# Optimization experiments

Measured on AMD Instinct MI355X. Metric: run time of the kernel, lower is better.

The kernel has to match this reference:

```python
import jax, jax.numpy as jnp
import numpy as np
from jax import lax

B, N, NCAM, NLVL = 2, 65536, 5, 3
CIN, MID, OUT, PTSC = 256, 128, 128, 128
H, W = 64, 112
EPS = 1e-3


def setup_inputs() -> dict:
    ks = jax.random.split(jax.random.key(0), 8)
    f32 = jnp.float32
    img_feats = jax.random.normal(ks[0], (NLVL, B * NCAM, CIN, H, W), f32)
    # points roughly in front of the cameras (z ~ 15) so many project in-bounds
    pts_xyz = jax.random.normal(ks[1], (B, N, 3), f32) * 10.0 + jnp.array([0.0, 0.0, 15.0], f32)
    cam_ids = jnp.sort(jax.random.randint(ks[2], (B, N), 0, NCAM), axis=1).astype(jnp.int32)
    pts_feats = jax.random.normal(ks[3], (B * N, PTSC), f32)
    T = jnp.broadcast_to(jnp.eye(4, dtype=f32), (NCAM, 4, 4))
    T = T.at[:, :3, 3].set(jax.random.normal(ks[4], (NCAM, 3), f32) * 0.5)
    fx, fy, cx, cy = 400.0, 400.0, 4.0 * W, 4.0 * H  # full-res intrinsics (feature stride 8)
    K = jnp.broadcast_to(jnp.array([[fx, 0.0, cx], [0.0, fy, cy], [0.0, 0.0, 1.0]], f32), (NCAM, 3, 3))
    conv_w = jax.random.normal(ks[5], (NLVL, MID, CIN, 3, 3), f32) * 0.02
    conv_b = jnp.zeros((NLVL, MID), f32)
    img_w = jax.random.normal(ks[6], (OUT, MID * NLVL), f32) * 0.05
    img_b = jnp.zeros((OUT,), f32)
    img_gamma = jnp.ones((OUT,), f32)
    img_beta = jnp.zeros((OUT,), f32)
    pts_w = jax.random.normal(ks[7], (OUT, PTSC), f32) * 0.05
    pts_b = jnp.zeros((OUT,), f32)
    pts_gamma = jnp.ones((OUT,), f32)
    pts_beta = jnp.zeros((OUT,), f32)
    return dict(img_feats=img_feats, pts_xyz=pts_xyz, pts_feats=pts_feats, T=T, K=K,
                conv_w=conv_w, conv_b=conv_b, img_w=img_w, img_b=img_b,
                img_gamma=img_gamma, img_beta=img_beta, pts_w=pts_w, pts_b=pts_b,
                pts_gamma=pts_gamma, pts_beta=pts_beta, cam_ids=cam_ids)


def _bn(x, gamma, beta):
    # BatchNorm1d in training mode: batch statistics, biased variance, eps=1e-3
    mu = jnp.mean(x, axis=0)
    var = jnp.var(x, axis=0)
    return (x - mu) * lax.rsqrt(var + EPS) * gamma + beta


def _bilinear(feat, bidx, cam, px, py):
    # feat: [B, NCAM, H, W, C]; px/py: [B, N] pixel coords (align_corners=True)
    # grid_sample bilinear with zeros padding: out-of-bounds corners contribute 0
    x0f = jnp.floor(px)
    y0f = jnp.floor(py)
    wx1 = px - x0f
    wy1 = py - y0f

    def corner(xf, yf, wgt):
        valid = (xf >= 0) & (xf <= W - 1) & (yf >= 0) & (yf <= H - 1)
        xi = jnp.clip(xf, 0, W - 1).astype(jnp.int32)
        yi = jnp.clip(yf, 0, H - 1).astype(jnp.int32)
        v = feat[bidx, cam, yi, xi]  # [B, N, C]
        return v * (wgt * valid)[..., None]

    return (corner(x0f, y0f, (1 - wx1) * (1 - wy1))
            + corner(x0f + 1, y0f, wx1 * (1 - wy1))
            + corner(x0f, y0f + 1, (1 - wx1) * wy1)
            + corner(x0f + 1, y0f + 1, wx1 * wy1))


def _forward(img_feats, pts_xyz, pts_feats, T, K, conv_w, conv_b, img_w, img_b,
             img_gamma, img_beta, pts_w, pts_b, pts_gamma, pts_beta, cam_ids):
    # scale intrinsics to the 1/8-resolution feature maps (K[0,0],K[0,2],K[1,1],K[1,2] /= 8)
    k_scale = jnp.array([[0.125, 1.0, 0.125], [1.0, 0.125, 0.125], [1.0, 1.0, 1.0]], jnp.float32)
    Ks = K * k_scale
    ones = jnp.ones(pts_xyz.shape[:2] + (1,), pts_xyz.dtype)
    xyz1 = jnp.concatenate([pts_xyz, ones], axis=-1)      # [B, N, 4]
    Tc = T[cam_ids]                                        # [B, N, 4, 4]
    Kc = Ks[cam_ids]                                       # [B, N, 3, 3]
    pc = jnp.einsum('bnij,bnj->bni', Tc, xyz1)[..., :3]    # camera-frame coords
    pim = jnp.einsum('bnij,bnj->bni', Kc, pc)
    uv = pim[..., :2] / pim[..., 2:3]
    gx = uv[..., 0] / W * 2.0 - 1.0                        # normalized grid coords
    gy = uv[..., 1] / H * 2.0 - 1.0
    px = (gx + 1.0) * 0.5 * (W - 1)                        # align_corners=True mapping
    py = (gy + 1.0) * 0.5 * (H - 1)
    bidx = jnp.broadcast_to(jnp.arange(B)[:, None], cam_ids.shape)
    lvl_feats = []
    for l in range(NLVL):
        f = lax.conv_general_dilated(img_feats[l], conv_w[l], (1, 1), 'SAME',
                                     dimension_numbers=('NCHW', 'OIHW', 'NCHW'))
        f = f + conv_b[l][None, :, None, None]
        f = f.reshape(B, NCAM, MID, H, W).transpose(0, 1, 3, 4, 2)  # [B,NCAM,H,W,C]
        lvl_feats.append(_bilinear(f, bidx, cam_ids, px, py))       # [B,N,MID]
    img_pts = jnp.concatenate(lvl_feats, axis=-1).reshape(B * N, MID * NLVL)
    img_pre = _bn(img_pts @ img_w.T + img_b, img_gamma, img_beta)
    pts_pre = _bn(pts_feats @ pts_w.T + pts_b, pts_gamma, pts_beta)
    return jax.nn.relu(img_pre + pts_pre)


def reference(img_feats, pts_xyz, pts_feats, T, K, conv_w, conv_b, img_w, img_b,
              img_gamma, img_beta, pts_w, pts_b, pts_gamma, pts_beta, cam_ids):
    return _forward(img_feats, pts_xyz, pts_feats, T, K, conv_w, conv_b, img_w, img_b,
                    img_gamma, img_beta, pts_w, pts_b, pts_gamma, pts_beta, cam_ids)
```

## Files before the change

kernel.cpp:

```cpp
#include <hip/hip_runtime.h>
#include <cstdint>

#define LVLPOS 75240
#define GUARD  256
#define NPART  16

using f32x4  = __attribute__((ext_vector_type(4))) float;
using bf16x8 = __attribute__((ext_vector_type(8))) __bf16;

static __device__ __forceinline__ unsigned short f2bf(float f) {
  unsigned int u = __float_as_uint(f);
  u += 0x7fffu + ((u >> 16) & 1u);
  return (unsigned short)(u >> 16);
}
static __device__ __forceinline__ float bflo(uint32_t d) { return __uint_as_float(d << 16); }
static __device__ __forceinline__ float bfhi(uint32_t d) { return __uint_as_float(d & 0xffff0000u); }

#define OFF_WF     ((size_t)0)
#define OFF_BIAS   ((size_t)1769472)
#define OFF_PTSWB  ((size_t)1769984)
#define OFF_STATSP ((size_t)1802752)
#define OFF_FDAT   ((size_t)1835520)
#define OFF_IMGP   ((size_t)21103104)
#define OFF_IRAW   OFF_IMGP
#define OFF_PRAW   (OFF_IMGP + (size_t)33554432)

__global__ __launch_bounds__(256) void k_setup(const float* __restrict__ img_w,
                                               const float* __restrict__ conv_w,
                                               const float* __restrict__ conv_b,
                                               const float* __restrict__ pts_w,
                                               unsigned short* __restrict__ wf,
                                               float* __restrict__ bias,
                                               unsigned short* __restrict__ pts_wb,
                                               unsigned short* __restrict__ imgP,
                                               float* __restrict__ statsP) {
  __shared__ float smem[12544];
  const int b = blockIdx.x, t = threadIdx.x;
  if (b < 432) {
    int z = b >> 1, oh = b & 1;
    int l = z / 72, r = z % 72, tap = r / 8, ckk = r % 8;
    float* iw = smem;
    float* cw = smem + 8320;
    for (int v = t; v < 2048; v += 256) {
      int o = v >> 5, seg = v & 31;
      float4 f = *(const float4*)(img_w + (size_t)(oh * 64 + o) * 384 + l * 128 + seg * 4);
      float* d = iw + o * 130 + seg * 4;
      d[0] = f.x; d[1] = f.y; d[2] = f.z; d[3] = f.w;
    }
    for (int v = t; v < 4096; v += 256) {
      int mid = v >> 5, cj = v & 31;
      cw[mid * 33 + cj] = conv_w[(size_t)((l * 128 + mid) * 256 + ckk * 32 + cj) * 9 + tap];
    }
    __syncthreads();
    const int o64 = t & 63, cs = t >> 6, o = oh * 64 + o64;
    float accs[8];
    #pragma unroll
    for (int ci = 0; ci < 8; ++ci) accs[ci] = 0.f;
    for (int mid = 0; mid < 128; ++mid) {
      float a = iw[o64 * 130 + mid];
      #pragma unroll
      for (int ci = 0; ci < 8; ++ci) accs[ci] = fmaf(a, cw[mid * 33 + cs * 8 + ci], accs[ci]);
    }
    #pragma unroll
    for (int ci = 0; ci < 8; ++ci) {
      int c = ckk * 32 + cs * 8 + ci;
      int ck64 = c >> 6, c64 = c & 63;
      int kh = c64 >> 5, kq3 = (c64 >> 3) & 3, el = c64 & 7;
      size_t idx = (size_t)((l * 4 + ck64) * 9 + tap) * 8192
                 + (size_t)(((o >> 4) * 2 + kh) * 512) + ((o & 15) + 16 * kq3) * 8 + el;
      wf[idx] = f2bf(accs[ci]);
    }
  } else if (b < 494) {
    int z = b - 432;
    size_t base; int n16;
    if (z == 60)      { base = 0; n16 = 8192; }
    else if (z == 61) { base = (size_t)(GUARD + 3 * LVLPOS) * 256; n16 = 8192; }
    else {
      int lvl = z / 20, w = z % 20, n = w >> 1, y = (w & 1) ? 65 : 0;
      base = (size_t)(GUARD + lvl * LVLPOS + (n * 66 + y) * 114) * 256; n16 = 3648;
    }
    uint4 zz = {0u, 0u, 0u, 0u};
    uint4* d = (uint4*)(imgP + base);
    for (int v = t; v < n16; v += 256) d[v] = zz;
  } else if (b < 559) {
    int z = b - 494;
    if (z == 0) {
      if (t < 128) {
        float a = 0.f;
        for (int i = 0; i < 384; ++i) a = fmaf(img_w[t * 384 + i], conv_b[i], a);
        bias[t] = a;
      }
    } else {
      int idx = (z - 1) * 256 + t;
      int o = idx >> 7, k = idx & 127;
      int ks = k >> 5, kq = (k >> 3) & 3, el = k & 7;
      int pos = (ks * 8 + (o >> 4)) * 512 + ((o & 15) + 16 * kq) * 8 + el;
      pts_wb[pos] = f2bf(pts_w[idx]);
    }
  } else {
    int z = b - 559;
    ((float4*)statsP)[z * 256 + t] = (float4){0.f, 0.f, 0.f, 0.f};
  }
}

__global__ __launch_bounds__(256) void k_nhwc(const float* __restrict__ img,
                                              unsigned short* __restrict__ imgP) {
  __shared__ unsigned short tile[256 * 114];
  const int t = threadIdx.x;
  const int lvl = blockIdx.x / 640, r = blockIdx.x % 640, n = r >> 6, y = r & 63;
  const float4* src4 = (const float4*)(img + (size_t)(lvl * 10 + n) * 1835008 + (size_t)y * 112);
  for (int v = t; v < 7168; v += 256) {
    int c = v / 28, s = v - c * 28;
    float4 f = src4[(size_t)c * 1792 + s];
    uint2 d;
    d.x = (uint32_t)f2bf(f.x) | ((uint32_t)f2bf(f.y) << 16);
    d.y = (uint32_t)f2bf(f.z) | ((uint32_t)f2bf(f.w) << 16);
    *(uint2*)(tile + c * 114 + s * 4) = d;
  }
  __syncthreads();
  uint32_t* dst = (uint32_t*)(imgP + (size_t)(GUARD + lvl * LVLPOS + (n * 66 + y + 1) * 114) * 256);
  for (int v = t; v < 14592; v += 256) {
    int xp = v >> 7, cp = v & 127;
    uint32_t val = 0;
    if (xp >= 1 && xp <= 112) {
      int x = xp - 1;
      val = (uint32_t)tile[(2 * cp) * 114 + x] | ((uint32_t)tile[(2 * cp + 1) * 114 + x] << 16);
    }
    dst[v] = val;
  }
}

#define APITCH 72
static __device__ __forceinline__ void conv_stage(unsigned short* dst,
                                                  const unsigned short* __restrict__ imgP,
                                                  int s, int m0, int t) {
  int lvl = s / 12, r = s - lvl * 12;
  int ck = r / 3, ky = r - ck * 3;
  const unsigned short* base = imgP
      + (size_t)(GUARD + lvl * LVLPOS + m0 - 1 + (ky - 1) * 114) * 256 + ck * 64;
  for (int v = t; v < 528; v += 256) {
    int p = v >> 3, seg = v & 7;
    *(uint4*)(dst + p * APITCH + seg * 8) = *(const uint4*)(base + (size_t)p * 256 + seg * 8);
  }
}

static __device__ __forceinline__ void conv_compute(const unsigned short* As_,
                                                    const unsigned short* __restrict__ wf,
                                                    int s, int mh, int nh, int m, int kq,
                                                    f32x4 (&acc)[2][4]) {
  const unsigned short* W0 = wf + (size_t)(3 * s) * 8192 + (nh * 8) * 512 + (m + 16 * kq) * 8;
  #pragma unroll
  for (int kx = 0; kx < 3; ++kx) {
    const unsigned short* Wp = W0 + kx * 8192;
    bf16x8 bv[4][2];
    #pragma unroll
    for (int nt = 0; nt < 4; ++nt) {
      bv[nt][0] = *(const bf16x8*)(Wp + (nt * 2) * 512);
      bv[nt][1] = *(const bf16x8*)(Wp + (nt * 2 + 1) * 512);
    }
    #pragma unroll
    for (int mt = 0; mt < 2; ++mt) {
      const unsigned short* ap = As_ + (mh * 32 + mt * 16 + m + kx) * APITCH + kq * 8;
      bf16x8 a0 = *(const bf16x8*)(ap);
      bf16x8 a1 = *(const bf16x8*)(ap + 32);
      #pragma unroll
      for (int nt = 0; nt < 4; ++nt) {
        acc[mt][nt] = __builtin_amdgcn_mfma_f32_16x16x32_bf16(a0, bv[nt][0], acc[mt][nt], 0, 0, 0);
        acc[mt][nt] = __builtin_amdgcn_mfma_f32_16x16x32_bf16(a1, bv[nt][1], acc[mt][nt], 0, 0, 0);
      }
    }
  }
}

__global__ __launch_bounds__(256, 4) void k_conv(const unsigned short* __restrict__ imgP,
                                                 const unsigned short* __restrict__ wf,
                                                 const float* __restrict__ bias,
                                                 unsigned short* __restrict__ fdat) {
  __shared__ unsigned short As[2][66 * APITCH];
  const int t = threadIdx.x, lane = t & 63, wave = t >> 6;
  const int mh = wave & 1, nh = wave >> 1;
  const int m = lane & 15, kq = lane >> 4;
  const int m0 = blockIdx.x * 64;

  f32x4 acc[2][4];
  #pragma unroll
  for (int i = 0; i < 2; ++i)
    #pragma unroll
    for (int j = 0; j < 4; ++j) acc[i][j] = (f32x4){0.f, 0.f, 0.f, 0.f};

  conv_stage(As[0], imgP, 0, m0, t);
  #pragma unroll 1
  for (int s = 0; s < 36; s += 2) {
    __syncthreads();
    if (s + 1 < 36) conv_stage(As[1], imgP, s + 1, m0, t);
    conv_compute(As[0], wf, s, mh, nh, m, kq, acc);
    __syncthreads();
    if (s + 2 < 36) conv_stage(As[0], imgP, s + 2, m0, t);
    conv_compute(As[1], wf, s + 1, mh, nh, m, kq, acc);
  }
  __syncthreads();

  unsigned short* Ep = &As[0][0];
  #pragma unroll
  for (int nt = 0; nt < 4; ++nt) {
    int oc = nh * 64 + nt * 16 + m;
    float bv = bias[oc];
    #pragma unroll
    for (int mt = 0; mt < 2; ++mt)
      #pragma unroll
      for (int rr = 0; rr < 4; ++rr)
        Ep[(mh * 32 + mt * 16 + kq * 4 + rr) * 128 + oc] = f2bf(acc[mt][nt][rr] + bv);
  }
  __syncthreads();
  unsigned short* dst = fdat + (size_t)m0 * 128;
  for (int v = t; v < 1024; v += 256)
    *(uint4*)(dst + v * 8) = *(const uint4*)(Ep + v * 8);
}

__global__ __launch_bounds__(256) void k_gp(const float* __restrict__ pts_xyz,
                                            const int* __restrict__ cam_ids,
                                            const float* __restrict__ Tm,
                                            const float* __restrict__ Km,
                                            const unsigned short* __restrict__ fdat,
                                            const float* __restrict__ pts_feats,
                                            const unsigned short* __restrict__ pts_wb,
                                            unsigned short* __restrict__ img_raw,
                                            unsigned short* __restrict__ pts_raw,
                                            float* __restrict__ statsP) {
  __shared__ __align__(16) char smem[36864];
  const int t = threadIdx.x, lane = t & 63, wave = t >> 6;

  if (blockIdx.x < 8192) {
    float* sb = (float*)smem;
    float* qb = sb + 128;
    if (t < 128) { sb[t] = 0.f; sb[128 + t] = 0.f; }
    __syncthreads();
    const int p0 = blockIdx.x * 16 + wave * 4;
    const uint32_t* fq = (const uint32_t*)fdat;
    float s0 = 0.f, q0 = 0.f, s1 = 0.f, q1 = 0.f;
    for (int j = 0; j < 4; ++j) {
      const int p = p0 + j;
      const int b = p >> 16;
      const int cam = cam_ids[p];
      const float X = pts_xyz[(size_t)p * 3], Y = pts_xyz[(size_t)p * 3 + 1], Z = pts_xyz[(size_t)p * 3 + 2];
      const float* Tc = Tm + cam * 16;
      float pcx = Tc[0] * X + Tc[1] * Y + Tc[2]  * Z + Tc[3];
      float pcy = Tc[4] * X + Tc[5] * Y + Tc[6]  * Z + Tc[7];
      float pcz = Tc[8] * X + Tc[9] * Y + Tc[10] * Z + Tc[11];
      const float* Kc = Km + cam * 9;
      float pimx = Kc[0] * 0.125f * pcx + Kc[1] * pcy          + Kc[2] * 0.125f * pcz;
      float pimy = Kc[3] * pcx          + Kc[4] * 0.125f * pcy + Kc[5] * 0.125f * pcz;
      float pimz = Kc[6] * pcx          + Kc[7] * pcy          + Kc[8] * pcz;
      float u = pimx / pimz, vv = pimy / pimz;
      float px = (u / 112.f) * 111.f;
      float py = (vv / 64.f) * 63.f;
      float x0 = floorf(px), y0 = floorf(py);
      float wx = px - x0, wy = py - y0;
      float cxf[4] = {x0, x0 + 1.f, x0, x0 + 1.f};
      float cyf[4] = {y0, y0, y0 + 1.f, y0 + 1.f};
      float cwt[4] = {(1.f - wx) * (1.f - wy), wx * (1.f - wy), (1.f - wx) * wy, wx * wy};
      const int nimg = b * 5 + cam;
      float wv[4]; int idx[4]; bool any = false;
      #pragma unroll
      for (int c4 = 0; c4 < 4; ++c4) {
        float xf = cxf[c4], yf = cyf[c4];
        bool valid = (xf >= 0.f) && (xf <= 111.f) && (yf >= 0.f) && (yf <= 63.f);
        float w = cwt[c4] * (valid ? 1.f : 0.f);
        int xi = (int)fminf(fmaxf(xf, 0.f), 111.f);
        int yi = (int)fminf(fmaxf(yf, 0.f), 63.f);
        wv[c4] = w;
        idx[c4] = (nimg * 66 + yi + 1) * 114 + xi + 1;
        any = any || (w != 0.f);
      }
      float a0 = 0.f, a1 = 0.f;
      if (any) {
        #pragma unroll
        for (int c4 = 0; c4 < 4; ++c4) {
          uint32_t d = fq[(size_t)idx[c4] * 64 + lane];
          a0 = fmaf(wv[c4], bflo(d), a0);
          a1 = fmaf(wv[c4], bfhi(d), a1);
        }
      }
      s0 += a0; q0 += a0 * a0; s1 += a1; q1 += a1 * a1;
      ((uint32_t*)img_raw)[(size_t)p * 64 + lane] =
          (uint32_t)f2bf(a0) | ((uint32_t)f2bf(a1) << 16);
    }
    atomicAdd(&sb[lane * 2], s0);
    atomicAdd(&sb[lane * 2 + 1], s1);
    atomicAdd(&qb[lane * 2], q0);
    atomicAdd(&qb[lane * 2 + 1], q1);
    __syncthreads();
    if (t < 128) {
      float* sp = statsP + (size_t)(blockIdx.x & (NPART - 1)) * 512;
      atomicAdd(sp + t, sb[t]);
      atomicAdd(sp + 128 + t, qb[t]);
    }
  } else {
    const int pb = blockIdx.x - 8192;
    const size_t r0 = (size_t)pb * 128;
    unsigned short* As2 = (unsigned short*)smem;
    const int mh = wave & 1, nh = wave >> 1;
    const int m = lane & 15, kq = lane >> 4;
    for (int v = t; v < 4096; v += 256) {
      int mm = v >> 5, seg = v & 31;
      float4 f = *(const float4*)(pts_feats + (r0 + mm) * 128 + seg * 4);
      uint2 d;
      d.x = (uint32_t)f2bf(f.x) | ((uint32_t)f2bf(f.y) << 16);
      d.y = (uint32_t)f2bf(f.z) | ((uint32_t)f2bf(f.w) << 16);
      *(uint2*)(As2 + mm * 136 + seg * 4) = d;
    }
    __syncthreads();
    f32x4 acc[4][4];
    #pragma unroll
    for (int i = 0; i < 4; ++i)
      #pragma unroll
      for (int jj = 0; jj < 4; ++jj) acc[i][jj] = (f32x4){0.f, 0.f, 0.f, 0.f};
    #pragma unroll
    for (int ks = 0; ks < 4; ++ks) {
      bf16x8 bv[4];
      #pragma unroll
      for (int nt = 0; nt < 4; ++nt)
        bv[nt] = *(const bf16x8*)(pts_wb + (size_t)((ks * 8 + nh * 4 + nt) * 512) + lane * 8);
      #pragma unroll
      for (int mt = 0; mt < 4; ++mt) {
        bf16x8 af = *(const bf16x8*)(As2 + (mh * 64 + mt * 16 + m) * 136 + ks * 32 + kq * 8);
        #pragma unroll
        for (int nt = 0; nt < 4; ++nt)
          acc[mt][nt] = __builtin_amdgcn_mfma_f32_16x16x32_bf16(af, bv[nt], acc[mt][nt], 0, 0, 0);
      }
    }
    __syncthreads();
    #pragma unroll
    for (int mt = 0; mt < 4; ++mt)
      #pragma unroll
      for (int nt = 0; nt < 4; ++nt)
        #pragma unroll
        for (int rr = 0; rr < 4; ++rr)
          As2[(mh * 64 + mt * 16 + kq * 4 + rr) * 128 + nh * 64 + nt * 16 + m] = f2bf(acc[mt][nt][rr]);
    __syncthreads();
    unsigned short* dst = pts_raw + r0 * 128;
    for (int v = t; v < 2048; v += 256)
      *(uint4*)(dst + v * 8) = *(const uint4*)(As2 + v * 8);
    float* ps = (float*)(smem + 34816);
    float* pq = ps + 256;
    pq = (float*)(smem + 35840);
    {
      int col = t & 127, rh = t >> 7;
      float s = 0.f, q = 0.f;
      for (int i = 0; i < 64; ++i) {
        float v = __uint_as_float((uint32_t)As2[(rh * 64 + i) * 128 + col] << 16);
        s += v; q += v * v;
      }
      ps[rh * 128 + col] = s;
      pq[rh * 128 + col] = q;
    }
    __syncthreads();
    if (t < 128) {
      float* sp = statsP + (size_t)(blockIdx.x & (NPART - 1)) * 512;
      atomicAdd(sp + 256 + t, ps[t] + ps[128 + t]);
      atomicAdd(sp + 384 + t, pq[t] + pq[128 + t]);
    }
  }
}

__global__ __launch_bounds__(256) void k_final(const unsigned short* __restrict__ img_raw,
                                               const unsigned short* __restrict__ pts_raw,
                                               const float* __restrict__ statsP,
                                               const float* __restrict__ img_gamma,
                                               const float* __restrict__ img_beta,
                                               const float* __restrict__ pts_gamma,
                                               const float* __restrict__ pts_beta,
                                               float* __restrict__ out) {
  __shared__ float sA[128], sB[128], sC[128];
  const int t = threadIdx.x;
  if (t < 128) {
    float si = 0.f, qi = 0.f, sp = 0.f, qp = 0.f;
    for (int k = 0; k < NPART; ++k) {
      const float* st = statsP + (size_t)k * 512;
      si += st[t]; qi += st[128 + t]; sp += st[256 + t]; qp += st[384 + t];
    }
    const float Nr = 131072.f;
    float mu_i = si / Nr;
    float var_i = qi / Nr - mu_i * mu_i;
    float a_i = img_gamma[t] * rsqrtf(var_i + 1e-3f);
    float mu_p = sp / Nr;
    float var_p = qp / Nr - mu_p * mu_p;
    float a_p = pts_gamma[t] * rsqrtf(var_p + 1e-3f);
    sA[t] = a_i; sB[t] = a_p;
    sC[t] = img_beta[t] + pts_beta[t] - a_i * mu_i - a_p * mu_p;
  }
  __syncthreads();
  const uint32_t* ir = (const uint32_t*)img_raw;
  const uint32_t* pr = (const uint32_t*)pts_raw;
  size_t g0 = (size_t)blockIdx.x * 2048;
  for (int i = 0; i < 8; ++i) {
    size_t g = g0 + i * 256 + t;
    uint32_t di = ir[g], dp = pr[g];
    int c = (int)(g & 63) * 2;
    float o0 = fmaxf(0.f, sA[c] * bflo(di) + sB[c] * bflo(dp) + sC[c]);
    float o1 = fmaxf(0.f, sA[c + 1] * bfhi(di) + sB[c + 1] * bfhi(dp) + sC[c + 1]);
    float2 o; o.x = o0; o.y = o1;
    *(float2*)(out + g * 2) = o;
  }
}

extern "C" void kernel_launch(void* const* d_in, const int* in_sizes, int n_in,
                              void* d_out, int out_size, void* d_ws, size_t ws_size,
                              hipStream_t stream) {
  const float* img_feats = (const float*)d_in[0];
  const float* pts_xyz   = (const float*)d_in[1];
  const float* pts_feats = (const float*)d_in[2];
  const float* Tm        = (const float*)d_in[3];
  const float* Km        = (const float*)d_in[4];
  const float* conv_w    = (const float*)d_in[5];
  const float* conv_b    = (const float*)d_in[6];
  const float* img_w     = (const float*)d_in[7];
  const float* img_gamma = (const float*)d_in[9];
  const float* img_beta  = (const float*)d_in[10];
  const float* pts_w     = (const float*)d_in[11];
  const float* pts_gamma = (const float*)d_in[13];
  const float* pts_beta  = (const float*)d_in[14];
  const int*   cam_ids   = (const int*)d_in[15];

  char* wsb = (char*)d_ws;
  unsigned short* wf      = (unsigned short*)(wsb + OFF_WF);
  float*          bias    = (float*)(wsb + OFF_BIAS);
  unsigned short* pts_wb  = (unsigned short*)(wsb + OFF_PTSWB);
  float*          statsP  = (float*)(wsb + OFF_STATSP);
  unsigned short* fdat    = (unsigned short*)(wsb + OFF_FDAT);
  unsigned short* imgP    = (unsigned short*)(wsb + OFF_IMGP);
  unsigned short* img_raw = (unsigned short*)(wsb + OFF_IRAW);
  unsigned short* pts_raw = (unsigned short*)(wsb + OFF_PRAW);

  k_setup<<<dim3(567), dim3(256), 0, stream>>>(img_w, conv_w, conv_b, pts_w,
                                               wf, bias, pts_wb, imgP, statsP);
  k_nhwc<<<dim3(1920), dim3(256), 0, stream>>>(img_feats, imgP);
  k_conv<<<dim3(1176), dim3(256), 0, stream>>>(imgP, wf, bias, fdat);
  k_gp<<<dim3(9216), dim3(256), 0, stream>>>(pts_xyz, cam_ids, Tm, Km, fdat,
                                             pts_feats, pts_wb, img_raw, pts_raw, statsP);
  k_final<<<dim3(4096), dim3(256), 0, stream>>>(img_raw, pts_raw, statsP,
                                                img_gamma, img_beta, pts_gamma, pts_beta,
                                                (float*)d_out);
}
```

Before: 742.3 us.

## Split conv per level with 128-row tiles and LDS-staged weights

The 3x3 conv kernel now gives each block a single level and 128 output rows, instead of accumulating all three levels into 64 rows. Weights are staged into double-buffered LDS with global_load_lds, so the MFMA loop reads B from shared memory rather than global. Per-level conv outputs and biases are now stored separately, and the gather kernel sums the three levels while sampling, which triples the gather read traffic and the fdat workspace. The NHWC transpose is split into channel halves using a padded 32-bit LDS tile, and the stats atomics in the gather are moved inside the per-point loop.

```diff
diff --git a/kernel.cpp b/kernel.cpp
--- a/kernel.cpp
+++ b/kernel.cpp
@@ -4,6 +4,7 @@
 #define LVLPOS 75240
 #define GUARD  256
 #define NPART  16
+#define FLVL32 4816896
 
 using f32x4  = __attribute__((ext_vector_type(4))) float;
 using bf16x8 = __attribute__((ext_vector_type(8))) __bf16;
@@ -16,12 +17,23 @@
 static __device__ __forceinline__ float bflo(uint32_t d) { return __uint_as_float(d << 16); }
 static __device__ __forceinline__ float bfhi(uint32_t d) { return __uint_as_float(d & 0xffff0000u); }
 
+#if __has_builtin(__builtin_amdgcn_global_load_lds)
+#define HAVE_GLL 1
+typedef const __attribute__((address_space(1))) unsigned int* gas1_t;
+typedef __attribute__((address_space(3))) unsigned int* las3_t;
+static __device__ __forceinline__ void gll16(const void* g, void* l) {
+  __builtin_amdgcn_global_load_lds((gas1_t)g, (las3_t)l, 16, 0, 0);
+}
+#else
+#define HAVE_GLL 0
+#endif
+
 #define OFF_WF     ((size_t)0)
 #define OFF_BIAS   ((size_t)1769472)
-#define OFF_PTSWB  ((size_t)1769984)
-#define OFF_STATSP ((size_t)1802752)
-#define OFF_FDAT   ((size_t)1835520)
-#define OFF_IMGP   ((size_t)21103104)
+#define OFF_PTSWB  ((size_t)1771008)
+#define OFF_STATSP ((size_t)1803776)
+#define OFF_FDAT   ((size_t)1836544)
+#define OFF_IMGP   ((size_t)59639296)
 #define OFF_IRAW   OFF_IMGP
 #define OFF_PRAW   (OFF_IMGP + (size_t)33554432)
 
@@ -86,9 +98,12 @@
     int z = b - 494;
     if (z == 0) {
       if (t < 128) {
-        float a = 0.f;
-        for (int i = 0; i < 384; ++i) a = fmaf(img_w[t * 384 + i], conv_b[i], a);
-        bias[t] = a;
+        for (int l = 0; l < 3; ++l) {
+          float a = 0.f;
+          for (int mid = 0; mid < 128; ++mid)
+            a = fmaf(img_w[t * 384 + l * 128 + mid], conv_b[l * 128 + mid], a);
+          bias[l * 128 + t] = a;
+        }
       }
     } else {
       int idx = (z - 1) * 256 + t;
@@ -105,115 +120,131 @@
 
 __global__ __launch_bounds__(256) void k_nhwc(const float* __restrict__ img,
                                               unsigned short* __restrict__ imgP) {
-  __shared__ unsigned short tile[256 * 114];
+  __shared__ uint32_t tile32[7280];
   const int t = threadIdx.x;
-  const int lvl = blockIdx.x / 640, r = blockIdx.x % 640, n = r >> 6, y = r & 63;
-  const float4* src4 = (const float4*)(img + (size_t)(lvl * 10 + n) * 1835008 + (size_t)y * 112);
-  for (int v = t; v < 7168; v += 256) {
-    int c = v / 28, s = v - c * 28;
-    float4 f = src4[(size_t)c * 1792 + s];
-    uint2 d;
-    d.x = (uint32_t)f2bf(f.x) | ((uint32_t)f2bf(f.y) << 16);
-    d.y = (uint32_t)f2bf(f.z) | ((uint32_t)f2bf(f.w) << 16);
-    *(uint2*)(tile + c * 114 + s * 4) = d;
+  const int lvl = blockIdx.x / 1280;
+  const int r = blockIdx.x % 1280;
+  const int n = r >> 7, w = r & 127, y = w >> 1, half = w & 1;
+  const float4* src4 = (const float4*)(img + (size_t)(lvl * 10 + n) * 1835008
+                                       + (size_t)(half * 128) * 7168 + (size_t)y * 112);
+  for (int v = t; v < 1792; v += 256) {
+    int s = v % 28, a = v / 28;
+    float4 f0 = src4[(size_t)(2 * a) * 1792 + s];
+    float4 f1 = src4[(size_t)(2 * a + 1) * 1792 + s];
+    uint32_t* dst = tile32 + (4 * s) * 65 + a;
+    dst[0]      = (uint32_t)f2bf(f0.x) | ((uint32_t)f2bf(f1.x) << 16);
+    dst[65]     = (uint32_t)f2bf(f0.y) | ((uint32_t)f2bf(f1.y) << 16);
+    dst[130]    = (uint32_t)f2bf(f0.z) | ((uint32_t)f2bf(f1.z) << 16);
+    dst[195]    = (uint32_t)f2bf(f0.w) | ((uint32_t)f2bf(f1.w) << 16);
   }
   __syncthreads();
-  uint32_t* dst = (uint32_t*)(imgP + (size_t)(GUARD + lvl * LVLPOS + (n * 66 + y + 1) * 114) * 256);
-  for (int v = t; v < 14592; v += 256) {
-    int xp = v >> 7, cp = v & 127;
+  uint32_t* dst32 = (uint32_t*)(imgP + (size_t)(GUARD + lvl * LVLPOS + (n * 66 + y + 1) * 114) * 256)
+                  + half * 64;
+  for (int v = t; v < 7296; v += 256) {
+    int xp = v >> 6, a = v & 63;
     uint32_t val = 0;
-    if (xp >= 1 && xp <= 112) {
-      int x = xp - 1;
-      val = (uint32_t)tile[(2 * cp) * 114 + x] | ((uint32_t)tile[(2 * cp + 1) * 114 + x] << 16);
-    }
-    dst[v] = val;
-  }
-}
-
-#define APITCH 72
-static __device__ __forceinline__ void conv_stage(unsigned short* dst,
-                                                  const unsigned short* __restrict__ imgP,
-                                                  int s, int m0, int t) {
-  int lvl = s / 12, r = s - lvl * 12;
-  int ck = r / 3, ky = r - ck * 3;
-  const unsigned short* base = imgP
-      + (size_t)(GUARD + lvl * LVLPOS + m0 - 1 + (ky - 1) * 114) * 256 + ck * 64;
-  for (int v = t; v < 528; v += 256) {
-    int p = v >> 3, seg = v & 7;
-    *(uint4*)(dst + p * APITCH + seg * 8) = *(const uint4*)(base + (size_t)p * 256 + seg * 8);
-  }
-}
-
-static __device__ __forceinline__ void conv_compute(const unsigned short* As_,
-                                                    const unsigned short* __restrict__ wf,
-                                                    int s, int mh, int nh, int m, int kq,
-                                                    f32x4 (&acc)[2][4]) {
-  const unsigned short* W0 = wf + (size_t)(3 * s) * 8192 + (nh * 8) * 512 + (m + 16 * kq) * 8;
-  #pragma unroll
-  for (int kx = 0; kx < 3; ++kx) {
-    const unsigned short* Wp = W0 + kx * 8192;
-    bf16x8 bv[4][2];
-    #pragma unroll
-    for (int nt = 0; nt < 4; ++nt) {
-      bv[nt][0] = *(const bf16x8*)(Wp + (nt * 2) * 512);
-      bv[nt][1] = *(const bf16x8*)(Wp + (nt * 2 + 1) * 512);
-    }
-    #pragma unroll
-    for (int mt = 0; mt < 2; ++mt) {
-      const unsigned short* ap = As_ + (mh * 32 + mt * 16 + m + kx) * APITCH + kq * 8;
-      bf16x8 a0 = *(const bf16x8*)(ap);
-      bf16x8 a1 = *(const bf16x8*)(ap + 32);
-      #pragma unroll
-      for (int nt = 0; nt < 4; ++nt) {
-        acc[mt][nt] = __builtin_amdgcn_mfma_f32_16x16x32_bf16(a0, bv[nt][0], acc[mt][nt], 0, 0, 0);
-        acc[mt][nt] = __builtin_amdgcn_mfma_f32_16x16x32_bf16(a1, bv[nt][1], acc[mt][nt], 0, 0, 0);
-      }
-    }
-  }
-}
-
-__global__ __launch_bounds__(256, 4) void k_conv(const unsigned short* __restrict__ imgP,
+    if (xp >= 1 && xp <= 112) val = tile32[(xp - 1) * 65 + a];
+    dst32[(size_t)xp * 128 + a] = val;
+  }
+}
+
+__global__ __launch_bounds__(256, 3) void k_conv(const unsigned short* __restrict__ imgP,
                                                  const unsigned short* __restrict__ wf,
                                                  const float* __restrict__ bias,
                                                  unsigned short* __restrict__ fdat) {
-  __shared__ unsigned short As[2][66 * APITCH];
+  __shared__ unsigned short lds[9360 + 2 * 8192];
+  unsigned short* As = lds;
+  unsigned short* Bs = lds + 9360;
   const int t = threadIdx.x, lane = t & 63, wave = t >> 6;
   const int mh = wave & 1, nh = wave >> 1;
   const int m = lane & 15, kq = lane >> 4;
-  const int m0 = blockIdx.x * 64;
-
-  f32x4 acc[2][4];
+  const int lvl = blockIdx.x / 588;
+  const int m0 = (blockIdx.x % 588) * 128;
+
+  f32x4 acc[4][4];
   #pragma unroll
-  for (int i = 0; i < 2; ++i)
+  for (int i = 0; i < 4; ++i)
     #pragma unroll
     for (int j = 0; j < 4; ++j) acc[i][j] = (f32x4){0.f, 0.f, 0.f, 0.f};
 
-  conv_stage(As[0], imgP, 0, m0, t);
+  const unsigned short* Alvl = imgP + ((size_t)GUARD + (size_t)lvl * LVLPOS + m0 - 1) * 256;
+  const unsigned short* Wlvl = wf + (size_t)lvl * 4 * 9 * 8192;
+
   #pragma unroll 1
-  for (int s = 0; s < 36; s += 2) {
-    __syncthreads();
-    if (s + 1 < 36) conv_stage(As[1], imgP, s + 1, m0, t);
-    conv_compute(As[0], wf, s, mh, nh, m, kq, acc);
-    __syncthreads();
-    if (s + 2 < 36) conv_stage(As[0], imgP, s + 2, m0, t);
-    conv_compute(As[1], wf, s + 1, mh, nh, m, kq, acc);
-  }
-  __syncthreads();
-
-  unsigned short* Ep = &As[0][0];
+  for (int s = 0; s < 12; ++s) {
+    const int ck = s >> 2 == 3 ? 3 : s / 3;
+    const int ck_ = s / 3, ky = s - ck_ * 3;
+    const unsigned short* Asrc = Alvl + (ptrdiff_t)(ky - 1) * 114 * 256 + ck_ * 64;
+    for (int v = t; v < 1040; v += 256) {
+      int p = v >> 3, seg = v & 7;
+      uint4 d = *(const uint4*)(Asrc + (size_t)p * 256 + seg * 8);
+      *(uint4*)(As + p * 72 + seg * 8) = d;
+    }
+    const unsigned short* Bsrc = Wlvl + (size_t)(ck_ * 9 + ky * 3) * 8192;
+#if HAVE_GLL
+    #pragma unroll
+    for (int i = 0; i < 4; ++i) {
+      int chunk = wave * 4 + i;
+      gll16(Bsrc + chunk * 512 + lane * 8, Bs + chunk * 512);
+    }
+#else
+    for (int v = t; v < 1024; v += 256)
+      *(uint4*)(Bs + v * 8) = *(const uint4*)(Bsrc + v * 8);
+#endif
+    __syncthreads();
+    #pragma unroll
+    for (int kx = 0; kx < 3; ++kx) {
+      if (kx < 2) {
+        const unsigned short* Bn = Bsrc + (kx + 1) * 8192;
+        unsigned short* Bd = Bs + ((kx + 1) & 1) * 8192;
+#if HAVE_GLL
+        #pragma unroll
+        for (int i = 0; i < 4; ++i) {
+          int chunk = wave * 4 + i;
+          gll16(Bn + chunk * 512 + lane * 8, Bd + chunk * 512);
+        }
+#else
+        for (int v = t; v < 1024; v += 256)
+          *(uint4*)(Bd + v * 8) = *(const uint4*)(Bn + v * 8);
+#endif
+      }
+      const unsigned short* Bb = Bs + (kx & 1) * 8192;
+      bf16x8 bfr[4][2];
+      #pragma unroll
+      for (int nt = 0; nt < 4; ++nt) {
+        const unsigned short* bp = Bb + ((nh * 4 + nt) * 2) * 512 + lane * 8;
+        bfr[nt][0] = *(const bf16x8*)(bp);
+        bfr[nt][1] = *(const bf16x8*)(bp + 512);
+      }
+      #pragma unroll
+      for (int mt = 0; mt < 4; ++mt) {
+        const unsigned short* ap = As + (mh * 64 + mt * 16 + m + kx) * 72 + kq * 8;
+        bf16x8 a0 = *(const bf16x8*)(ap);
+        bf16x8 a1 = *(const bf16x8*)(ap + 32);
+        #pragma unroll
+        for (int nt = 0; nt < 4; ++nt) {
+          acc[mt][nt] = __builtin_amdgcn_mfma_f32_16x16x32_bf16(a0, bfr[nt][0], acc[mt][nt], 0, 0, 0);
+          acc[mt][nt] = __builtin_amdgcn_mfma_f32_16x16x32_bf16(a1, bfr[nt][1], acc[mt][nt], 0, 0, 0);
+        }
+      }
+      __syncthreads();
+    }
+  }
+
+  unsigned short* Ep = lds;
   #pragma unroll
   for (int nt = 0; nt < 4; ++nt) {
     int oc = nh * 64 + nt * 16 + m;
-    float bv = bias[oc];
-    #pragma unroll
-    for (int mt = 0; mt < 2; ++mt)
+    float bv = bias[lvl * 128 + oc];
+    #pragma unroll
+    for (int mt = 0; mt < 4; ++mt)
       #pragma unroll
       for (int rr = 0; rr < 4; ++rr)
-        Ep[(mh * 32 + mt * 16 + kq * 4 + rr) * 128 + oc] = f2bf(acc[mt][nt][rr] + bv);
+        Ep[(mh * 64 + mt * 16 + kq * 4 + rr) * 128 + oc] = f2bf(acc[mt][nt][rr] + bv);
   }
   __syncthreads();
-  unsigned short* dst = fdat + (size_t)m0 * 128;
-  for (int v = t; v < 1024; v += 256)
+  unsigned short* dst = fdat + (size_t)lvl * 9633792 + (size_t)m0 * 128;
+  for (int v = t; v < 2048; v += 256)
     *(uint4*)(dst + v * 8) = *(const uint4*)(Ep + v * 8);
 }
 
@@ -237,7 +268,6 @@
     __syncthreads();
     const int p0 = blockIdx.x * 16 + wave * 4;
     const uint32_t* fq = (const uint32_t*)fdat;
-    float s0 = 0.f, q0 = 0.f, s1 = 0.f, q1 = 0.f;
     for (int j = 0; j < 4; ++j) {
       const int p = p0 + j;
       const int b = p >> 16;
@@ -276,19 +306,24 @@
       if (any) {
         #pragma unroll
         for (int c4 = 0; c4 < 4; ++c4) {
-          uint32_t d = fq[(size_t)idx[c4] * 64 + lane];
-          a0 = fmaf(wv[c4], bflo(d), a0);
-          a1 = fmaf(wv[c4], bfhi(d), a1);
+          const uint32_t* q = fq + (size_t)idx[c4] * 64 + lane;
+          float w = wv[c4];
+          #pragma unroll
+          for (int lv = 0; lv < 3; ++lv) {
+            uint32_t d = q[(size_t)lv * FLVL32];
+            a0 = fmaf(w, bflo(d), a0);
+            a1 = fmaf(w, bfhi(d), a1);
+          }
         }
       }
-      s0 += a0; q0 += a0 * a0; s1 += a1; q1 += a1 * a1;
+      float s0 = a0, q0 = a0 * a0, s1 = a1, q1 = a1 * a1;
+      atomicAdd(&sb[lane * 2], s0);
+      atomicAdd(&sb[lane * 2 + 1], s1);
+      atomicAdd(&qb[lane * 2], q0);
+      atomicAdd(&qb[lane * 2 + 1], q1);
       ((uint32_t*)img_raw)[(size_t)p * 64 + lane] =
           (uint32_t)f2bf(a0) | ((uint32_t)f2bf(a1) << 16);
     }
-    atomicAdd(&sb[lane * 2], s0);
-    atomicAdd(&sb[lane * 2 + 1], s1);
-    atomicAdd(&qb[lane * 2], q0);
-    atomicAdd(&qb[lane * 2 + 1], q1);
     __syncthreads();
     if (t < 128) {
       float* sp = statsP + (size_t)(blockIdx.x & (NPART - 1)) * 512;
@@ -342,8 +377,7 @@
     for (int v = t; v < 2048; v += 256)
       *(uint4*)(dst + v * 8) = *(const uint4*)(As2 + v * 8);
     float* ps = (float*)(smem + 34816);
-    float* pq = ps + 256;
-    pq = (float*)(smem + 35840);
+    float* pq = (float*)(smem + 35840);
     {
       int col = t & 127, rh = t >> 7;
       float s = 0.f, q = 0.f;
@@ -434,8 +468,8 @@
 
   k_setup<<<dim3(567), dim3(256), 0, stream>>>(img_w, conv_w, conv_b, pts_w,
                                                wf, bias, pts_wb, imgP, statsP);
-  k_nhwc<<<dim3(1920), dim3(256), 0, stream>>>(img_feats, imgP);
-  k_conv<<<dim3(1176), dim3(256), 0, stream>>>(imgP, wf, bias, fdat);
+  k_nhwc<<<dim3(3840), dim3(256), 0, stream>>>(img_feats, imgP);
+  k_conv<<<dim3(1764), dim3(256), 0, stream>>>(imgP, wf, bias, fdat);
   k_gp<<<dim3(9216), dim3(256), 0, stream>>>(pts_xyz, cam_ids, Tm, Km, fdat,
                                              pts_feats, pts_wb, img_raw, pts_raw, statsP);
   k_final<<<dim3(4096), dim3(256), 0, stream>>>(img_raw, pts_raw, statsP,
```

New measurement: 758.8 us. 1.02x slower.
